# Performance work log

Measured on AMD Instinct MI355X. Metric: run time of the kernel, lower is better.

The kernel has to match this reference:

```python
import jax, jax.numpy as jnp
import numpy as np

IN_FEATURES = 4096
RANK = 64
NUM_EXPERTS = 8
ALPHA = 64.0
SPARSITY = 0.8
SCALING = ALPHA / RANK  # alpha / rank


def setup_inputs() -> dict:
    key = jax.random.key(0)
    k1, k2, k3, k4 = jax.random.split(key, 4)
    B, S = 4, 4096
    projected_input = jax.random.normal(k1, (B, S, RANK), dtype=jnp.float32)
    routing_weights = jax.random.uniform(k2, (B, S, NUM_EXPERTS), dtype=jnp.float32)
    # Stacked expert A matrices [K, in_features, rank] (kaiming-like init ~ normal here)
    A = jax.random.normal(k3, (NUM_EXPERTS, IN_FEATURES, RANK), dtype=jnp.float32) * 0.02
    sparse_mask = (jax.random.uniform(k4, (NUM_EXPERTS, IN_FEATURES, RANK)) >= SPARSITY).astype(jnp.float32)
    A = A * sparse_mask  # module masks A at init as well
    return {
        "projected_input": projected_input,
        "routing_weights": routing_weights,
        "A": A,
        "sparse_mask": sparse_mask,
    }


def reference(projected_input, routing_weights, A, sparse_mask):
    # A_sparse[k] = A[k] * mask[k]; per expert: scaling * (p @ A_sparse[k].T)
    # then weighted sum over experts with routing_weights[..., k].
    A_eff = (A * sparse_mask) * SCALING          # [k, d, r]
    # Weight the rank-projected input per expert, then contract:
    # wp[b,s,k,r] = routing_weights[b,s,k] * projected_input[b,s,r]
    wp = jnp.einsum("bsk,bsr->bskr", routing_weights, projected_input)
    out = jnp.einsum("bskr,kdr->bsd", wp, A_eff)  # [b, s, in_features]
    return out
```

## Files before the change

kernel.cpp:

```cpp
#include <hip/hip_runtime.h>

#define IN_FEATURES 4096
#define RANK 64
#define NUM_EXPERTS 8
#define KDIM 512
#define TOKENS 16384
#define SCALING 1.0f

#define BM 128
#define BN 128
#define BK 64

typedef __bf16 bf16x8 __attribute__((ext_vector_type(8)));
typedef float f32x4 __attribute__((ext_vector_type(4)));

__device__ __forceinline__ unsigned short f2bf(float f) {
  union { float f; unsigned int u; } v; v.f = f;
  unsigned int u = v.u;
  u += 0x7fffu + ((u >> 16) & 1u);
  return (unsigned short)(u >> 16);
}

__device__ __forceinline__ void gload_lds16(const unsigned short* g, unsigned short* l) {
  __builtin_amdgcn_global_load_lds(
      (const __attribute__((address_space(1))) void*)g,
      (__attribute__((address_space(3))) void*)l,
      16, 0, 0);
}

__global__ void __launch_bounds__(256) q_pack(const float* __restrict__ p,
                                              const float* __restrict__ w,
                                              unsigned short* __restrict__ q) {
  int t = blockIdx.x;
  int i = threadIdx.x;
  int k = i >> 5;
  int rp = (i & 31) * 2;
  float wk = w[t * NUM_EXPERTS + k];
  float p0 = p[t * RANK + rp];
  float p1 = p[t * RANK + rp + 1];
  ushort2 o;
  o.x = f2bf(wk * p0);
  o.y = f2bf(wk * p1);
  *(ushort2*)&q[t * KDIM + k * RANK + rp] = o;
}

__global__ void __launch_bounds__(256) b_pack(const float* __restrict__ A,
                                              const float* __restrict__ mask,
                                              unsigned short* __restrict__ Bt) {
  int d = blockIdx.x;
  int i = threadIdx.x;
  int k = i >> 5;
  int rp = (i & 31) * 2;
  long src = ((long)k * IN_FEATURES + d) * RANK + rp;
  float a0 = A[src] * mask[src] * SCALING;
  float a1 = A[src + 1] * mask[src + 1] * SCALING;
  ushort2 o;
  o.x = f2bf(a0);
  o.y = f2bf(a1);
  *(ushort2*)&Bt[d * KDIM + k * RANK + rp] = o;
}

__global__ void __launch_bounds__(256, 2) gemm_kernel(
    const unsigned short* __restrict__ q,
    const unsigned short* __restrict__ Bt,
    float* __restrict__ out) {
  __shared__ __align__(16) unsigned short sA[BM * BK];
  __shared__ __align__(16) unsigned short sB[BN * BK];

  const int tid = threadIdx.x;
  const int lane = tid & 63;
  const int wid = tid >> 6;
  const int u = lane & 15;
  const int quad = lane >> 4;
  const int wave_m = (wid >> 1) * 64;
  const int wave_n = (wid & 1) * 64;

  const int m0 = blockIdx.y * BM;
  const int n0 = blockIdx.x * BN;

  f32x4 acc[4][4];
#pragma unroll
  for (int i = 0; i < 4; ++i)
#pragma unroll
    for (int j = 0; j < 4; ++j)
      acc[i][j] = (f32x4){0.f, 0.f, 0.f, 0.f};

  const unsigned short* gA[4];
  const unsigned short* gB[4];
  unsigned short* lA[4];
  unsigned short* lB[4];
#pragma unroll
  for (int j = 0; j < 4; ++j) {
    int c = j * 256 + tid;
    int row = c >> 3;
    int logc = (c & 7) ^ (row & 7);
    gA[j] = q  + (long)(m0 + row) * KDIM + logc * 8;
    gB[j] = Bt + (long)(n0 + row) * KDIM + logc * 8;
    lA[j] = sA + c * 8;
    lB[j] = sB + c * 8;
  }

  for (int kt = 0; kt < KDIM; kt += BK) {
#pragma unroll
    for (int j = 0; j < 4; ++j) {
      gload_lds16(gA[j] + kt, lA[j]);
      gload_lds16(gB[j] + kt, lB[j]);
    }
    __syncthreads();

#pragma unroll
    for (int ki = 0; ki < 2; ++ki) {
      bf16x8 af[4], bfr[4];
      const int physbase = ki * 4;
#pragma unroll
      for (int mi = 0; mi < 4; ++mi) {
        int row = wave_m + mi * 16 + u;
        int phys = (physbase + quad) ^ (u & 7);
        af[mi] = *(const bf16x8*)&sA[row * BK + phys * 8];
      }
#pragma unroll
      for (int ni = 0; ni < 4; ++ni) {
        int row = wave_n + ni * 16 + u;
        int phys = (physbase + quad) ^ (u & 7);
        bfr[ni] = *(const bf16x8*)&sB[row * BK + phys * 8];
      }
#pragma unroll
      for (int mi = 0; mi < 4; ++mi)
#pragma unroll
        for (int ni = 0; ni < 4; ++ni)
          acc[mi][ni] = __builtin_amdgcn_mfma_f32_16x16x32_bf16(
              af[mi], bfr[ni], acc[mi][ni], 0, 0, 0);
    }
    __syncthreads();
  }

#pragma unroll
  for (int mi = 0; mi < 4; ++mi) {
#pragma unroll
    for (int r = 0; r < 4; ++r) {
      int row = m0 + wave_m + mi * 16 + quad * 4 + r;
#pragma unroll
      for (int ni = 0; ni < 4; ++ni) {
        int col = n0 + wave_n + ni * 16 + u;
        out[(long)row * IN_FEATURES + col] = acc[mi][ni][r];
      }
    }
  }
}

extern "C" void kernel_launch(void* const* d_in, const int* in_sizes, int n_in,
                              void* d_out, int out_size, void* d_ws, size_t ws_size,
                              hipStream_t stream) {
  const float* p    = (const float*)d_in[0];
  const float* w    = (const float*)d_in[1];
  const float* A    = (const float*)d_in[2];
  const float* mask = (const float*)d_in[3];
  float* out = (float*)d_out;

  unsigned short* q  = (unsigned short*)d_ws;
  unsigned short* Bt = q + (size_t)TOKENS * KDIM;

  q_pack<<<TOKENS, 256, 0, stream>>>(p, w, q);
  b_pack<<<IN_FEATURES, 256, 0, stream>>>(A, mask, Bt);

  dim3 grid(IN_FEATURES / BN, TOKENS / BM);
  gemm_kernel<<<grid, dim3(256), 0, stream>>>(q, Bt, out);
}
```

Before: 328.2 us.

## Merge pack kernels into one launch and swap GEMM grid ordering

Merges the q and B packing kernels into a single launch, with each token-block now handling four tokens, which removes one kernel launch and its tail. The GEMM grid is transposed so blockIdx.x walks M tiles, which changes which tiles run at the same time and so the L2 reuse pattern. The launch_bounds occupancy hint of 2 is dropped, which may change register allocation and occupancy.

After: 348.3 us. 1.06x slower.

```diff
diff --git a/kernel.cpp b/kernel.cpp
--- a/kernel.cpp
+++ b/kernel.cpp
@@ -28,39 +28,36 @@
       16, 0, 0);
 }
 
-__global__ void __launch_bounds__(256) q_pack(const float* __restrict__ p,
-                                              const float* __restrict__ w,
-                                              unsigned short* __restrict__ q) {
-  int t = blockIdx.x;
+__global__ void __launch_bounds__(256) pack_kernel(
+    const float* __restrict__ p, const float* __restrict__ w,
+    const float* __restrict__ A, const float* __restrict__ mask,
+    unsigned short* __restrict__ q, unsigned short* __restrict__ Bt) {
+  int b = blockIdx.x;
   int i = threadIdx.x;
   int k = i >> 5;
   int rp = (i & 31) * 2;
-  float wk = w[t * NUM_EXPERTS + k];
-  float p0 = p[t * RANK + rp];
-  float p1 = p[t * RANK + rp + 1];
-  ushort2 o;
-  o.x = f2bf(wk * p0);
-  o.y = f2bf(wk * p1);
-  *(ushort2*)&q[t * KDIM + k * RANK + rp] = o;
+  if (b < IN_FEATURES) {
+    int d = b;
+    long src = ((long)k * IN_FEATURES + d) * RANK + rp;
+    float a0 = A[src] * mask[src] * SCALING;
+    float a1 = A[src + 1] * mask[src + 1] * SCALING;
+    ushort2 o; o.x = f2bf(a0); o.y = f2bf(a1);
+    *(ushort2*)&Bt[d * KDIM + k * RANK + rp] = o;
+  } else {
+    int t0 = (b - IN_FEATURES) * 4;
+#pragma unroll
+    for (int s = 0; s < 4; ++s) {
+      int t = t0 + s;
+      float wk = w[t * NUM_EXPERTS + k];
+      float p0 = p[t * RANK + rp];
+      float p1 = p[t * RANK + rp + 1];
+      ushort2 o; o.x = f2bf(wk * p0); o.y = f2bf(wk * p1);
+      *(ushort2*)&q[t * KDIM + k * RANK + rp] = o;
+    }
+  }
 }
 
-__global__ void __launch_bounds__(256) b_pack(const float* __restrict__ A,
-                                              const float* __restrict__ mask,
-                                              unsigned short* __restrict__ Bt) {
-  int d = blockIdx.x;
-  int i = threadIdx.x;
-  int k = i >> 5;
-  int rp = (i & 31) * 2;
-  long src = ((long)k * IN_FEATURES + d) * RANK + rp;
-  float a0 = A[src] * mask[src] * SCALING;
-  float a1 = A[src + 1] * mask[src + 1] * SCALING;
-  ushort2 o;
-  o.x = f2bf(a0);
-  o.y = f2bf(a1);
-  *(ushort2*)&Bt[d * KDIM + k * RANK + rp] = o;
-}
-
-__global__ void __launch_bounds__(256, 2) gemm_kernel(
+__global__ void __launch_bounds__(256) gemm_kernel(
     const unsigned short* __restrict__ q,
     const unsigned short* __restrict__ Bt,
     float* __restrict__ out) {
@@ -75,8 +72,8 @@
   const int wave_m = (wid >> 1) * 64;
   const int wave_n = (wid & 1) * 64;
 
-  const int m0 = blockIdx.y * BM;
-  const int n0 = blockIdx.x * BN;
+  const int m0 = blockIdx.x * BM;
+  const int n0 = blockIdx.y * BN;
 
   f32x4 acc[4][4];
 #pragma unroll
@@ -160,9 +157,8 @@
   unsigned short* q  = (unsigned short*)d_ws;
   unsigned short* Bt = q + (size_t)TOKENS * KDIM;
 
-  q_pack<<<TOKENS, 256, 0, stream>>>(p, w, q);
-  b_pack<<<IN_FEATURES, 256, 0, stream>>>(A, mask, Bt);
+  pack_kernel<<<IN_FEATURES + TOKENS / 4, 256, 0, stream>>>(p, w, A, mask, q, Bt);
 
-  dim3 grid(IN_FEATURES / BN, TOKENS / BM);
+  dim3 grid(TOKENS / BM, IN_FEATURES / BN);
   gemm_kernel<<<grid, dim3(256), 0, stream>>>(q, Bt, out);
 }
```
